# Kernel tuning notes

Hardware: AMD Instinct MI355X
Metric: run time of the kernel (lower is better)

Reference implementation:

```python
import jax, jax.numpy as jnp
import numpy as np


def setup_inputs() -> dict:
    key = jax.random.key(0)
    k1, k2, k3, k4 = jax.random.split(key, 4)
    E = 1_600_000
    N = 100_000
    IN, OUT = 128, 256
    edge_index = jax.random.randint(k1, (2, E), 0, N, dtype=jnp.int32)
    time_encoding = jax.random.normal(k2, (E, IN), dtype=jnp.float32)
    # Linear(in_channels, out_channels): weight [OUT, IN], bias [OUT]
    bound = 1.0 / np.sqrt(IN)
    W = jax.random.uniform(k3, (OUT, IN), minval=-bound, maxval=bound, dtype=jnp.float32)
    b = jax.random.uniform(k4, (OUT,), minval=-bound, maxval=bound, dtype=jnp.float32)
    return {"edge_index": edge_index, "time_encoding": time_encoding,
            "num_nodes": N, "W": W, "b": b}


def reference(edge_index, time_encoding, num_nodes, W, b):
    # scatter-add per-edge time encodings into destination-node buckets
    col = edge_index[1]
    agg = jax.ops.segment_sum(time_encoding, col, num_segments=num_nodes)  # [N, IN]
    # dense projection: Linear -> x @ W.T + b
    return agg @ W.T + b  # [N, OUT]
```

## Files before the change

kernel.cpp:

```cpp
#include <hip/hip_runtime.h>
#include <hip/hip_bf16.h>

#define IN_CH 128
#define OUT_CH 256
#define BLK_SCAN 1024

typedef __bf16 bf16x8 __attribute__((ext_vector_type(8)));
typedef float f32x4 __attribute__((ext_vector_type(4)));

__device__ inline unsigned short f2bf(float f) {
  union { float f; unsigned int u; } v; v.f = f;
  unsigned int u = v.u;
  u += 0x7FFFu + ((u >> 16) & 1u);
  return (unsigned short)(u >> 16);
}

__global__ void init_kernel(const float* __restrict__ W, unsigned short* __restrict__ Bpack,
                            int* __restrict__ count, int N) {
  int i = blockIdx.x * blockDim.x + threadIdx.x;
  if (i < N) count[i] = 0;
  if (i < IN_CH * OUT_CH) {
    const int j  = i & 7;
    const int c  = (i >> 3) & 15;
    const int kb = (i >> 7) & 3;
    const int ks = (i >> 9) & 3;
    const int tn = i >> 11;
    const int row = tn * 16 + c;
    const int k   = ks * 32 + kb * 8 + j;
    Bpack[i] = f2bf(W[(size_t)row * IN_CH + k]);
  }
}

__global__ void hist_kernel(const int* __restrict__ col, int E, int* __restrict__ count) {
  int i = blockIdx.x * blockDim.x + threadIdx.x;
  int b = i * 4;
  if (b + 4 <= E) {
    const int4 c = *(const int4*)(col + b);
    atomicAdd(&count[c.x], 1);
    atomicAdd(&count[c.y], 1);
    atomicAdd(&count[c.z], 1);
    atomicAdd(&count[c.w], 1);
  } else {
    for (int j = b; j < E; ++j) atomicAdd(&count[col[j]], 1);
  }
}

__global__ __launch_bounds__(BLK_SCAN) void scan_block_kernel(
    const int* __restrict__ count, int N, int* __restrict__ excl, int* __restrict__ bsum) {
  __shared__ int wsum[16];
  const int tid = threadIdx.x;
  const int i = blockIdx.x * BLK_SCAN + tid;
  const int v = (i < N) ? count[i] : 0;
  int x = v;
#pragma unroll
  for (int d = 1; d < 64; d <<= 1) {
    int t = __shfl_up(x, d, 64);
    if ((tid & 63) >= d) x += t;
  }
  if ((tid & 63) == 63) wsum[tid >> 6] = x;
  __syncthreads();
  if (tid < 16) {
    int s = wsum[tid];
#pragma unroll
    for (int d = 1; d < 16; d <<= 1) {
      int t = __shfl_up(s, d, 16);
      if (tid >= d) s += t;
    }
    wsum[tid] = s;
  }
  __syncthreads();
  const int w = tid >> 6;
  const int prefix = (w == 0) ? 0 : wsum[w - 1];
  if (i < N) excl[i] = prefix + x - v;
  if (tid == BLK_SCAN - 1) bsum[blockIdx.x] = prefix + x;
}

__global__ void scan_bsum_kernel(int* __restrict__ bsum, int nb) {
  __shared__ int tmp[256];
  const int tid = threadIdx.x;
  int run = 0;
  for (int s = 0; s < nb; s += 256) {
    int v = (s + tid < nb) ? bsum[s + tid] : 0;
    tmp[tid] = v;
    __syncthreads();
    for (int d = 1; d < 256; d <<= 1) {
      int t = (tid >= d) ? tmp[tid - d] : 0;
      __syncthreads();
      tmp[tid] += t;
      __syncthreads();
    }
    if (s + tid < nb) bsum[s + tid] = run + tmp[tid] - v;
    run += tmp[255];
    __syncthreads();
  }
}

__global__ void add_offsets_kernel(int* __restrict__ excl, const int* __restrict__ bsum,
                                   int* __restrict__ cursor, int N) {
  int i = blockIdx.x * blockDim.x + threadIdx.x;
  if (i < N) {
    int o = excl[i] + bsum[i / BLK_SCAN];
    excl[i] = o;
    cursor[i] = o;
  }
}

__global__ void scatter_kernel(const int* __restrict__ col, int E,
                               int* __restrict__ cursor, int* __restrict__ sorted) {
  int i = blockIdx.x * blockDim.x + threadIdx.x;
  int b = i * 4;
  if (b + 4 <= E) {
    const int4 c = *(const int4*)(col + b);
    int p0 = atomicAdd(&cursor[c.x], 1); sorted[p0] = b;
    int p1 = atomicAdd(&cursor[c.y], 1); sorted[p1] = b + 1;
    int p2 = atomicAdd(&cursor[c.z], 1); sorted[p2] = b + 2;
    int p3 = atomicAdd(&cursor[c.w], 1); sorted[p3] = b + 3;
  } else {
    for (int j = b; j < E; ++j) {
      int pos = atomicAdd(&cursor[col[j]], 1);
      sorted[pos] = j;
    }
  }
}

__global__ __launch_bounds__(256) void aggregate_kernel(
    const float* __restrict__ te, const int* __restrict__ offsets,
    const int* __restrict__ cend, const int* __restrict__ sorted,
    unsigned int* __restrict__ aggb32, int N) {
  const int g    = threadIdx.x >> 6;
  const int lane = threadIdx.x & 63;
  const int n = blockIdx.x * 4 + g;
  if (n >= N) return;

  float ax = 0.f, ay = 0.f;
  const int s = offsets[n];
  const int e = cend[n];
  const size_t co = (size_t)(lane * 2);
  if (s < e) {
    int my = 0;
    if (lane < 16) {
      int idx = s + lane;
      my = sorted[idx < e ? idx : (e - 1)];
    }
    for (int i = s; i < e; i += 16) {
#define EID(j) __builtin_amdgcn_readlane(my, j)
      const float2 t0  = *(const float2*)(te + (size_t)EID(0)  * IN_CH + co);
      const float2 t1  = *(const float2*)(te + (size_t)EID(1)  * IN_CH + co);
      const float2 t2  = *(const float2*)(te + (size_t)EID(2)  * IN_CH + co);
      const float2 t3  = *(const float2*)(te + (size_t)EID(3)  * IN_CH + co);
      const float2 t4  = *(const float2*)(te + (size_t)EID(4)  * IN_CH + co);
      const float2 t5  = *(const float2*)(te + (size_t)EID(5)  * IN_CH + co);
      const float2 t6  = *(const float2*)(te + (size_t)EID(6)  * IN_CH + co);
      const float2 t7  = *(const float2*)(te + (size_t)EID(7)  * IN_CH + co);
      const float2 t8  = *(const float2*)(te + (size_t)EID(8)  * IN_CH + co);
      const float2 t9  = *(const float2*)(te + (size_t)EID(9)  * IN_CH + co);
      const float2 t10 = *(const float2*)(te + (size_t)EID(10) * IN_CH + co);
      const float2 t11 = *(const float2*)(te + (size_t)EID(11) * IN_CH + co);
      const float2 t12 = *(const float2*)(te + (size_t)EID(12) * IN_CH + co);
      const float2 t13 = *(const float2*)(te + (size_t)EID(13) * IN_CH + co);
      const float2 t14 = *(const float2*)(te + (size_t)EID(14) * IN_CH + co);
      const float2 t15 = *(const float2*)(te + (size_t)EID(15) * IN_CH + co);
#undef EID
      int nxt = 0;
      {
        const int ib = i + 16;
        if (lane < 16 && ib < e) {
          int idx = ib + lane;
          nxt = sorted[idx < e ? idx : (e - 1)];
        }
      }
      const int rem = e - i;
      if (rem >= 16) {
        ax += (t0.x + t1.x) + (t2.x + t3.x) + (t4.x + t5.x) + (t6.x + t7.x) +
              (t8.x + t9.x) + (t10.x + t11.x) + (t12.x + t13.x) + (t14.x + t15.x);
        ay += (t0.y + t1.y) + (t2.y + t3.y) + (t4.y + t5.y) + (t6.y + t7.y) +
              (t8.y + t9.y) + (t10.y + t11.y) + (t12.y + t13.y) + (t14.y + t15.y);
      } else {
        ax += t0.x; ay += t0.y;
#define ACC(j, tj) { const float c = (rem > j) ? 1.f : 0.f; \
                     ax = fmaf(c, tj.x, ax); ay = fmaf(c, tj.y, ay); }
        ACC(1, t1)  ACC(2, t2)  ACC(3, t3)  ACC(4, t4)  ACC(5, t5)
        ACC(6, t6)  ACC(7, t7)  ACC(8, t8)  ACC(9, t9)  ACC(10, t10)
        ACC(11, t11) ACC(12, t12) ACC(13, t13) ACC(14, t14) ACC(15, t15)
#undef ACC
      }
      my = nxt;
    }
  }
  aggb32[(size_t)n * 64 + lane] = (unsigned int)f2bf(ax) | ((unsigned int)f2bf(ay) << 16);
}

__global__ __launch_bounds__(256) void project_mfma(
    const unsigned short* __restrict__ aggb, const unsigned short* __restrict__ Bpack,
    const float* __restrict__ bias, float* __restrict__ out, int N) {
  const int wave = threadIdx.x >> 6;
  const int lane = threadIdx.x & 63;
  const int r  = lane & 15;
  const int kb = lane >> 4;
  const int m0 = blockIdx.x * 16;

  bf16x8 a[4];
  const unsigned short* arow = aggb + (size_t)(m0 + r) * IN_CH + kb * 8;
#pragma unroll
  for (int ks = 0; ks < 4; ++ks)
    a[ks] = *(const bf16x8*)(arow + ks * 32);

  f32x4 acc[4];
#pragma unroll
  for (int ct = 0; ct < 4; ++ct) acc[ct] = (f32x4){0.f, 0.f, 0.f, 0.f};

#pragma unroll
  for (int ct = 0; ct < 4; ++ct) {
    const int tn = wave * 4 + ct;
#pragma unroll
    for (int ks = 0; ks < 4; ++ks) {
      const bf16x8 b = *(const bf16x8*)(Bpack + (size_t)((((tn * 4 + ks) * 4 + kb) * 16 + r) * 8));
      acc[ct] = __builtin_amdgcn_mfma_f32_16x16x32_bf16(a[ks], b, acc[ct], 0, 0, 0);
    }
  }

#pragma unroll
  for (int ct = 0; ct < 4; ++ct) {
    const int col = wave * 64 + ct * 16 + r;
    const float bv = bias[col];
#pragma unroll
    for (int j = 0; j < 4; ++j) {
      const int m = m0 + kb * 4 + j;
      if (m < N) out[(size_t)m * OUT_CH + col] = acc[ct][j] + bv;
    }
  }
}

extern "C" void kernel_launch(void* const* d_in, const int* in_sizes, int n_in,
                              void* d_out, int out_size, void* d_ws, size_t ws_size,
                              hipStream_t stream) {
  const int* edge_index = (const int*)d_in[0];
  const float* te       = (const float*)d_in[1];
  const float* W        = (const float*)d_in[3];
  const float* bias     = (const float*)d_in[4];
  float* out            = (float*)d_out;

  const int E = in_sizes[0] / 2;
  const int N = out_size / OUT_CH;
  const int* col = edge_index + E;

  const int Np = (N + 3) & ~3;
  const int Ep = (E + 3) & ~3;
  int* ws      = (int*)d_ws;
  int* count   = ws;
  int* offsets = ws + Np;
  int* cursor  = ws + 2 * Np;
  int* bsum    = ws + 3 * Np;
  int* sorted  = ws + 3 * Np + 4096;
  unsigned short* Bpack = (unsigned short*)(ws + 3 * Np + 4096 + Ep);
  unsigned int*   aggb  = (unsigned int*)(ws + 3 * Np + 4096 + Ep + 16384);

  const int nb = (N + BLK_SCAN - 1) / BLK_SCAN;
  const int init_n = (N > IN_CH * OUT_CH) ? N : IN_CH * OUT_CH;

  hipLaunchKernelGGL(init_kernel, dim3((init_n + 255) / 256), dim3(256), 0, stream,
                     W, Bpack, count, N);
  hipLaunchKernelGGL(hist_kernel, dim3((E / 4 + 255) / 256), dim3(256), 0, stream, col, E, count);
  hipLaunchKernelGGL(scan_block_kernel, dim3(nb), dim3(BLK_SCAN), 0, stream, count, N, offsets, bsum);
  hipLaunchKernelGGL(scan_bsum_kernel, dim3(1), dim3(256), 0, stream, bsum, nb);
  hipLaunchKernelGGL(add_offsets_kernel, dim3((N + 255) / 256), dim3(256), 0, stream,
                     offsets, bsum, cursor, N);
  hipLaunchKernelGGL(scatter_kernel, dim3((E / 4 + 255) / 256), dim3(256), 0, stream,
                     col, E, cursor, sorted);
  hipLaunchKernelGGL(aggregate_kernel, dim3((N + 3) / 4), dim3(256), 0, stream,
                     te, offsets, cursor, sorted, aggb, N);
  hipLaunchKernelGGL(project_mfma, dim3((N + 15) / 16), dim3(256), 0, stream,
                     (const unsigned short*)aggb, Bpack, bias, out, N);
}
```

Measured before the change: 438.6 us.

## Bin edges into 16-node buckets and fuse aggregation with MFMA projection

Replaces the per-node counting sort with coarse bucketing by groups of 16 destination nodes. Each edge's time-encoding row is streamed once, coarsely, into a bucket-ordered bf16 buffer, instead of being gathered at random per node. A fused phase2 kernel then accumulates each bucket's rows into shared memory with LDS atomics and immediately runs the MFMA projection, removing the intermediate aggregate round trip and two launches. The trade-off is an extra full write and read of the bf16 binned copy (about 400MB of workspace) and the precision loss from rounding each edge to bf16 before summation. The old path is kept as a fallback when workspace is too small.

```diff
diff --git a/kernel.cpp b/kernel.cpp
--- a/kernel.cpp
+++ b/kernel.cpp
@@ -4,6 +4,8 @@
 #define IN_CH 128
 #define OUT_CH 256
 #define BLK_SCAN 1024
+#define BUCKET_SHIFT 4
+#define BNODES 16
 
 typedef __bf16 bf16x8 __attribute__((ext_vector_type(8)));
 typedef float f32x4 __attribute__((ext_vector_type(4)));
@@ -15,34 +17,21 @@
   return (unsigned short)(u >> 16);
 }
 
-__global__ void init_kernel(const float* __restrict__ W, unsigned short* __restrict__ Bpack,
-                            int* __restrict__ count, int N) {
+__device__ inline void build_bpack_elem(const float* __restrict__ W,
+                                        unsigned short* __restrict__ Bpack, int i) {
+  const int j  = i & 7;
+  const int c  = (i >> 3) & 15;
+  const int kb = (i >> 7) & 3;
+  const int ks = (i >> 9) & 3;
+  const int tn = i >> 11;
+  Bpack[i] = f2bf(W[(size_t)(tn * 16 + c) * IN_CH + ks * 32 + kb * 8 + j]);
+}
+
+__global__ void initB_kernel(const float* __restrict__ W, unsigned short* __restrict__ Bpack,
+                             int* __restrict__ cnt, int nzero) {
   int i = blockIdx.x * blockDim.x + threadIdx.x;
-  if (i < N) count[i] = 0;
-  if (i < IN_CH * OUT_CH) {
-    const int j  = i & 7;
-    const int c  = (i >> 3) & 15;
-    const int kb = (i >> 7) & 3;
-    const int ks = (i >> 9) & 3;
-    const int tn = i >> 11;
-    const int row = tn * 16 + c;
-    const int k   = ks * 32 + kb * 8 + j;
-    Bpack[i] = f2bf(W[(size_t)row * IN_CH + k]);
-  }
-}
-
-__global__ void hist_kernel(const int* __restrict__ col, int E, int* __restrict__ count) {
-  int i = blockIdx.x * blockDim.x + threadIdx.x;
-  int b = i * 4;
-  if (b + 4 <= E) {
-    const int4 c = *(const int4*)(col + b);
-    atomicAdd(&count[c.x], 1);
-    atomicAdd(&count[c.y], 1);
-    atomicAdd(&count[c.z], 1);
-    atomicAdd(&count[c.w], 1);
-  } else {
-    for (int j = b; j < E; ++j) atomicAdd(&count[col[j]], 1);
-  }
+  if (i < nzero) cnt[i] = 0;
+  if (i < IN_CH * OUT_CH) build_bpack_elem(W, Bpack, i);
 }
 
 __global__ __launch_bounds__(BLK_SCAN) void scan_block_kernel(
@@ -105,8 +94,145 @@
   }
 }
 
-__global__ void scatter_kernel(const int* __restrict__ col, int E,
-                               int* __restrict__ cursor, int* __restrict__ sorted) {
+
+__global__ void hist_bucket_kernel(const int* __restrict__ col, int E, int* __restrict__ cnt) {
+  int i = blockIdx.x * blockDim.x + threadIdx.x;
+  int b = i * 4;
+  if (b + 4 <= E) {
+    const int4 c = *(const int4*)(col + b);
+    atomicAdd(&cnt[c.x >> BUCKET_SHIFT], 1);
+    atomicAdd(&cnt[c.y >> BUCKET_SHIFT], 1);
+    atomicAdd(&cnt[c.z >> BUCKET_SHIFT], 1);
+    atomicAdd(&cnt[c.w >> BUCKET_SHIFT], 1);
+  } else {
+    for (int j = b; j < E; ++j) atomicAdd(&cnt[col[j] >> BUCKET_SHIFT], 1);
+  }
+}
+
+__global__ __launch_bounds__(256) void bin_kernel(
+    const float* __restrict__ te, const int* __restrict__ col,
+    int* __restrict__ cursor, unsigned int* __restrict__ binned,
+    int* __restrict__ bnid, int E) {
+  const int lane = threadIdx.x & 63;
+  const int gw = (blockIdx.x * 256 + threadIdx.x) >> 6;
+  const int nw = (gridDim.x * 256) >> 6;
+  for (int base = gw * 4; base < E; base += nw * 4) {
+    int ne = E - base; if (ne > 4) ne = 4;
+    int mypos = 0;
+    if (lane < ne) {
+      const int c = col[base + lane];
+      mypos = atomicAdd(&cursor[c >> BUCKET_SHIFT], 1);
+      bnid[mypos] = c & (BNODES - 1);
+    }
+#pragma unroll
+    for (int j = 0; j < 4; ++j) {
+      if (j < ne) {
+        const int pos = __builtin_amdgcn_readlane(mypos, j);
+        const float lo = te[(size_t)(base + j) * IN_CH + lane];
+        const float hi = te[(size_t)(base + j) * IN_CH + lane + 64];
+        binned[(size_t)pos * 64 + lane] =
+            (unsigned int)f2bf(lo) | ((unsigned int)f2bf(hi) << 16);
+      }
+    }
+  }
+}
+
+__global__ __launch_bounds__(256) void phase2_kernel(
+    const unsigned int* __restrict__ binned, const int* __restrict__ bnid,
+    const int* __restrict__ start, const int* __restrict__ cend,
+    const unsigned short* __restrict__ Bpack, const float* __restrict__ bias,
+    float* __restrict__ out, int N) {
+  __shared__ float agg[BNODES][IN_CH];
+  const int tid = threadIdx.x;
+  const int wave = tid >> 6;
+  const int lane = tid & 63;
+  const int b = blockIdx.x;
+  const int s = start[b];
+  const int e = cend[b];
+
+#pragma unroll
+  for (int i = tid; i < BNODES * IN_CH; i += 256) ((float*)agg)[i] = 0.f;
+  __syncthreads();
+
+  for (int r0 = s + wave * 4; r0 < e; r0 += 16) {
+    int nr = e - r0; if (nr > 4) nr = 4;
+    unsigned int v[4]; int nid[4];
+#pragma unroll
+    for (int j = 0; j < 4; ++j) {
+      if (j < nr) {
+        v[j] = binned[(size_t)(r0 + j) * 64 + lane];
+        nid[j] = bnid[r0 + j];
+      }
+    }
+#pragma unroll
+    for (int j = 0; j < 4; ++j) {
+      if (j < nr) {
+        union { unsigned int u; float f; } lo, hi;
+        lo.u = v[j] << 16;
+        hi.u = v[j] & 0xFFFF0000u;
+        atomicAdd(&agg[nid[j]][lane], lo.f);
+        atomicAdd(&agg[nid[j]][lane + 64], hi.f);
+      }
+    }
+  }
+  __syncthreads();
+
+  const int r  = lane & 15;
+  const int kb = lane >> 4;
+  const int m0 = b * BNODES;
+
+  bf16x8 a[4];
+#pragma unroll
+  for (int ks = 0; ks < 4; ++ks) {
+    bf16x8 t;
+#pragma unroll
+    for (int j = 0; j < 8; ++j) t[j] = (__bf16)agg[r][ks * 32 + kb * 8 + j];
+    a[ks] = t;
+  }
+
+  f32x4 acc[4];
+#pragma unroll
+  for (int ct = 0; ct < 4; ++ct) acc[ct] = (f32x4){0.f, 0.f, 0.f, 0.f};
+
+#pragma unroll
+  for (int ct = 0; ct < 4; ++ct) {
+    const int tn = wave * 4 + ct;
+#pragma unroll
+    for (int ks = 0; ks < 4; ++ks) {
+      const bf16x8 bb = *(const bf16x8*)(Bpack + (size_t)((((tn * 4 + ks) * 4 + kb) * 16 + r) * 8));
+      acc[ct] = __builtin_amdgcn_mfma_f32_16x16x32_bf16(a[ks], bb, acc[ct], 0, 0, 0);
+    }
+  }
+
+#pragma unroll
+  for (int ct = 0; ct < 4; ++ct) {
+    const int colo = wave * 64 + ct * 16 + r;
+    const float bv = bias[colo];
+#pragma unroll
+    for (int j = 0; j < 4; ++j) {
+      const int m = m0 + kb * 4 + j;
+      if (m < N) out[(size_t)m * OUT_CH + colo] = acc[ct][j] + bv;
+    }
+  }
+}
+
+
+__global__ void fb_hist_kernel(const int* __restrict__ col, int E, int* __restrict__ count) {
+  int i = blockIdx.x * blockDim.x + threadIdx.x;
+  int b = i * 4;
+  if (b + 4 <= E) {
+    const int4 c = *(const int4*)(col + b);
+    atomicAdd(&count[c.x], 1);
+    atomicAdd(&count[c.y], 1);
+    atomicAdd(&count[c.z], 1);
+    atomicAdd(&count[c.w], 1);
+  } else {
+    for (int j = b; j < E; ++j) atomicAdd(&count[col[j]], 1);
+  }
+}
+
+__global__ void fb_scatter_kernel(const int* __restrict__ col, int E,
+                                  int* __restrict__ cursor, int* __restrict__ sorted) {
   int i = blockIdx.x * blockDim.x + threadIdx.x;
   int b = i * 4;
   if (b + 4 <= E) {
@@ -123,7 +249,7 @@
   }
 }
 
-__global__ __launch_bounds__(256) void aggregate_kernel(
+__global__ __launch_bounds__(256) void fb_aggregate_kernel(
     const float* __restrict__ te, const int* __restrict__ offsets,
     const int* __restrict__ cend, const int* __restrict__ sorted,
     unsigned int* __restrict__ aggb32, int N) {
@@ -190,7 +316,7 @@
   aggb32[(size_t)n * 64 + lane] = (unsigned int)f2bf(ax) | ((unsigned int)f2bf(ay) << 16);
 }
 
-__global__ __launch_bounds__(256) void project_mfma(
+__global__ __launch_bounds__(256) void fb_project_mfma(
     const unsigned short* __restrict__ aggb, const unsigned short* __restrict__ Bpack,
     const float* __restrict__ bias, float* __restrict__ out, int N) {
   const int wave = threadIdx.x >> 6;
@@ -198,9 +324,10 @@
   const int r  = lane & 15;
   const int kb = lane >> 4;
   const int m0 = blockIdx.x * 16;
+  const int rr = (m0 + r < N) ? (m0 + r) : (N - 1);
 
   bf16x8 a[4];
-  const unsigned short* arow = aggb + (size_t)(m0 + r) * IN_CH + kb * 8;
+  const unsigned short* arow = aggb + (size_t)rr * IN_CH + kb * 8;
 #pragma unroll
   for (int ks = 0; ks < 4; ++ks)
     a[ks] = *(const bf16x8*)(arow + ks * 32);
@@ -214,22 +341,23 @@
     const int tn = wave * 4 + ct;
 #pragma unroll
     for (int ks = 0; ks < 4; ++ks) {
-      const bf16x8 b = *(const bf16x8*)(Bpack + (size_t)((((tn * 4 + ks) * 4 + kb) * 16 + r) * 8));
-      acc[ct] = __builtin_amdgcn_mfma_f32_16x16x32_bf16(a[ks], b, acc[ct], 0, 0, 0);
+      const bf16x8 bb = *(const bf16x8*)(Bpack + (size_t)((((tn * 4 + ks) * 4 + kb) * 16 + r) * 8));
+      acc[ct] = __builtin_amdgcn_mfma_f32_16x16x32_bf16(a[ks], bb, acc[ct], 0, 0, 0);
     }
   }
 
 #pragma unroll
   for (int ct = 0; ct < 4; ++ct) {
-    const int col = wave * 64 + ct * 16 + r;
-    const float bv = bias[col];
+    const int colo = wave * 64 + ct * 16 + r;
+    const float bv = bias[colo];
 #pragma unroll
     for (int j = 0; j < 4; ++j) {
       const int m = m0 + kb * 4 + j;
-      if (m < N) out[(size_t)m * OUT_CH + col] = acc[ct][j] + bv;
-    }
-  }
-}
+      if (m < N) out[(size_t)m * OUT_CH + colo] = acc[ct][j] + bv;
+    }
+  }
+}
+
 
 extern "C" void kernel_launch(void* const* d_in, const int* in_sizes, int n_in,
                               void* d_out, int out_size, void* d_ws, size_t ws_size,
@@ -244,31 +372,66 @@
   const int N = out_size / OUT_CH;
   const int* col = edge_index + E;
 
+  const int K = (N + BNODES - 1) >> BUCKET_SHIFT;
+  const int Kp = (K + 3) & ~3;
+  const int Ep = (E + 3) & ~3;
+
+  char* p = (char*)d_ws;
+  unsigned short* Bpack = (unsigned short*)p;      p += 65536;
+  int* cnt    = (int*)p;                           p += (size_t)Kp * 4;
+  int* start  = (int*)p;                           p += (size_t)Kp * 4;
+  int* cursor = (int*)p;                           p += (size_t)Kp * 4;
+  int* bsum   = (int*)p;                           p += 4096 * 4;
+  int* bnid   = (int*)p;                           p += (size_t)Ep * 4;
+  p = (char*)(((uintptr_t)p + 255) & ~(uintptr_t)255);
+  unsigned int* binned = (unsigned int*)p;         p += (size_t)E * 256;
+  const size_t need_primary = (size_t)(p - (char*)d_ws);
+
+  if (ws_size >= need_primary) {
+    const int nb = (K + BLK_SCAN - 1) / BLK_SCAN;
+    const int init_n = (K > IN_CH * OUT_CH) ? K : IN_CH * OUT_CH;
+    hipLaunchKernelGGL(initB_kernel, dim3((init_n + 255) / 256), dim3(256), 0, stream,
+                       W, Bpack, cnt, K);
+    hipLaunchKernelGGL(hist_bucket_kernel, dim3((E / 4 + 255) / 256), dim3(256), 0, stream,
+                       col, E, cnt);
+    hipLaunchKernelGGL(scan_block_kernel, dim3(nb), dim3(BLK_SCAN), 0, stream,
+                       cnt, K, start, bsum);
+    hipLaunchKernelGGL(scan_bsum_kernel, dim3(1), dim3(256), 0, stream, bsum, nb);
+    hipLaunchKernelGGL(add_offsets_kernel, dim3((K + 255) / 256), dim3(256), 0, stream,
+                       start, bsum, cursor, K);
+    hipLaunchKernelGGL(bin_kernel, dim3(2048), dim3(256), 0, stream,
+                       te, col, cursor, binned, bnid, E);
+    hipLaunchKernelGGL(phase2_kernel, dim3(K), dim3(256), 0, stream,
+                       binned, bnid, start, cursor, Bpack, bias, out, N);
+    return;
+  }
+
   const int Np = (N + 3) & ~3;
-  const int Ep = (E + 3) & ~3;
-  int* ws      = (int*)d_ws;
-  int* count   = ws;
-  int* offsets = ws + Np;
-  int* cursor  = ws + 2 * Np;
-  int* bsum    = ws + 3 * Np;
-  int* sorted  = ws + 3 * Np + 4096;
-  unsigned short* Bpack = (unsigned short*)(ws + 3 * Np + 4096 + Ep);
-  unsigned int*   aggb  = (unsigned int*)(ws + 3 * Np + 4096 + Ep + 16384);
-
-  const int nb = (N + BLK_SCAN - 1) / BLK_SCAN;
+  int* ws       = (int*)d_ws;
+  int* fcount   = ws;
+  int* foffsets = ws + Np;
+  int* fcursor  = ws + 2 * Np;
+  int* fbsum    = ws + 3 * Np;
+  int* fsorted  = ws + 3 * Np + 4096;
+  unsigned short* fBpack = (unsigned short*)(ws + 3 * Np + 4096 + Ep);
+  unsigned int*   faggb  = (unsigned int*)(ws + 3 * Np + 4096 + Ep + 16384);
+
+  const int nbf = (N + BLK_SCAN - 1) / BLK_SCAN;
   const int init_n = (N > IN_CH * OUT_CH) ? N : IN_CH * OUT_CH;
 
-  hipLaunchKernelGGL(init_kernel, dim3((init_n + 255) / 256), dim3(256), 0, stream,
-                     W, Bpack, count, N);
-  hipLaunchKernelGGL(hist_kernel, dim3((E / 4 + 255) / 256), dim3(256), 0, stream, col, E, count);
-  hipLaunchKernelGGL(scan_block_kernel, dim3(nb), dim3(BLK_SCAN), 0, stream, count, N, offsets, bsum);
-  hipLaunchKernelGGL(scan_bsum_kernel, dim3(1), dim3(256), 0, stream, bsum, nb);
+  hipLaunchKernelGGL(initB_kernel, dim3((init_n + 255) / 256), dim3(256), 0, stream,
+                     W, fBpack, fcount, N);
+  hipLaunchKernelGGL(fb_hist_kernel, dim3((E / 4 + 255) / 256), dim3(256), 0, stream,
+                     col, E, fcount);
+  hipLaunchKernelGGL(scan_block_kernel, dim3(nbf), dim3(BLK_SCAN), 0, stream,
+                     fcount, N, foffsets, fbsum);
+  hipLaunchKernelGGL(scan_bsum_kernel, dim3(1), dim3(256), 0, stream, fbsum, nbf);
   hipLaunchKernelGGL(add_offsets_kernel, dim3((N + 255) / 256), dim3(256), 0, stream,
-                     offsets, bsum, cursor, N);
-  hipLaunchKernelGGL(scatter_kernel, dim3((E / 4 + 255) / 256), dim3(256), 0, stream,
-                     col, E, cursor, sorted);
-  hipLaunchKernelGGL(aggregate_kernel, dim3((N + 3) / 4), dim3(256), 0, stream,
-                     te, offsets, cursor, sorted, aggb, N);
-  hipLaunchKernelGGL(project_mfma, dim3((N + 15) / 16), dim3(256), 0, stream,
-                     (const unsigned short*)aggb, Bpack, bias, out, N);
-}
+                     foffsets, fbsum, fcursor, N);
+  hipLaunchKernelGGL(fb_scatter_kernel, dim3((E / 4 + 255) / 256), dim3(256), 0, stream,
+                     col, E, fcursor, fsorted);
+  hipLaunchKernelGGL(fb_aggregate_kernel, dim3((N + 3) / 4), dim3(256), 0, stream,
+                     te, foffsets, fcursor, fsorted, faggb, N);
+  hipLaunchKernelGGL(fb_project_mfma, dim3((N + 15) / 16), dim3(256), 0, stream,
+                     (const unsigned short*)faggb, fBpack, bias, out, N);
+}
```

Result: slower. 1.435 ms (+227.2%).
